# Kernel optimization log

Hardware: AMD Instinct MI355X
Metric: run time of the kernel (lower is better)

## Reference

```python
import jax, jax.numpy as jnp
import numpy as np

B, T, E = 2, 2048, 1024
H = 16
D = E // H  # 64

def setup_inputs() -> dict:
    key = jax.random.key(0)
    kx, kq, kk, kv, ko = jax.random.split(key, 5)
    s = 1.0 / np.sqrt(E)
    return {
        "x":  jax.random.normal(kx, (B, T, E), dtype=jnp.float32),
        "Wq": jax.random.normal(kq, (E, E), dtype=jnp.float32) * s,
        "Wk": jax.random.normal(kk, (E, E), dtype=jnp.float32) * s,
        "Wv": jax.random.normal(kv, (E, E), dtype=jnp.float32) * s,
        "Wo": jax.random.normal(ko, (E, E), dtype=jnp.float32) * s,
    }

def reference(x, Wq, Wk, Wv, Wo):
    # Faithful to the torch module, including its quirks:
    #  - head split is a raw .view(B, H, T, D) reshape (NOT a transpose split)
    #  - masked_fill result is discarded in the original, so NO causal mask is applied
    #  - dropout = 0.0 -> identity
    b, t, e = x.shape
    q = jnp.reshape(x @ Wq, (b, H, t, D))
    k = jnp.reshape(x @ Wk, (b, H, t, D))
    v = jnp.reshape(x @ Wv, (b, H, t, D))
    # raw_score = q @ k^T ; softmax over keys of raw_score / sqrt(head_dim)
    scores = jnp.einsum("bhtd,bhsd->bhts", q, k) / jnp.sqrt(jnp.asarray(D, x.dtype))
    attn = jax.nn.softmax(scores, axis=-1)
    h = jnp.einsum("bhts,bhsd->bhtd", attn, v)           # (B,H,T,D)
    h = jnp.reshape(h, (b, t, e))                         # .view(B, T, -1)
    return h @ Wo
```

## Files before the change

### kernel.cpp

```cpp
#include <hip/hip_runtime.h>
#include <hip/hip_bf16.h>
#include <math.h>

#define BB 2
#define TT 2048
#define EE 1024
#define HH 16
#define DD 64
#define MM (BB*TT)

typedef __bf16 bf16;
typedef bf16 bf16x8 __attribute__((ext_vector_type(8)));
typedef bf16 bf16x4 __attribute__((ext_vector_type(4)));
typedef bf16 bf16x2 __attribute__((ext_vector_type(2)));
typedef float f32x4 __attribute__((ext_vector_type(4)));

#define MFMA16(a,b,c) __builtin_amdgcn_mfma_f32_16x16x32_bf16((a),(b),(c),0,0,0)

__device__ __forceinline__ void gload_lds16(const void* g, void* l) {
  __builtin_amdgcn_global_load_lds(
      (const __attribute__((address_space(1))) unsigned int*)g,
      (__attribute__((address_space(3))) unsigned int*)l, 16, 0, 0);
}

__device__ __forceinline__ unsigned short bits(bf16 h) {
  return __builtin_bit_cast(unsigned short, h);
}

__global__ __launch_bounds__(256) void cvt_bf16(const float* __restrict__ in,
                                                bf16* __restrict__ out, int n4) {
  int i = blockIdx.x * blockDim.x + threadIdx.x;
  if (i < n4) {
    float4 f = ((const float4*)in)[i];
    bf16x4 h;
    h[0] = (bf16)f.x; h[1] = (bf16)f.y; h[2] = (bf16)f.z; h[3] = (bf16)f.w;
    ((bf16x4*)out)[i] = h;
  }
}

__global__ __launch_bounds__(256) void transpose_cvt4(const float* __restrict__ w0,
                                                      const float* __restrict__ w1,
                                                      const float* __restrict__ w2,
                                                      const float* __restrict__ w3,
                                                      bf16* t0, bf16* t1, bf16* t2, bf16* t3) {
  const float* W = blockIdx.z == 0 ? w0 : blockIdx.z == 1 ? w1 : blockIdx.z == 2 ? w2 : w3;
  bf16* T = blockIdx.z == 0 ? t0 : blockIdx.z == 1 ? t1 : blockIdx.z == 2 ? t2 : t3;
  __shared__ bf16 tile[64][65];
  const int n0 = blockIdx.x * 64, k0 = blockIdx.y * 64;
#pragma unroll
  for (int i = 0; i < 16; i++) {
    int idx = threadIdx.x + i * 256;
    int r = idx >> 6, c = idx & 63;
    tile[c][r] = (bf16)W[(size_t)(k0 + r) * EE + n0 + c];
  }
  __syncthreads();
#pragma unroll
  for (int i = 0; i < 16; i++) {
    int idx = threadIdx.x + i * 256;
    int r = idx >> 6, c = idx & 63;
    T[(size_t)(n0 + r) * EE + k0 + c] = tile[r][c];
  }
}

template <typename OutT>
__device__ __forceinline__ void gemm_core(const bf16* __restrict__ A, const bf16* __restrict__ Bt,
                                          OutT* __restrict__ C, bf16* As, bf16* Bs) {
  const int tid = threadIdx.x;
  const int w = tid >> 6, lane = tid & 63;
  const int lg = lane >> 4, lr = lane & 15;
  const int row0 = blockIdx.y * 128, col0 = blockIdx.x * 128;
  const int wrow = (w >> 1) * 64, wcol = (w & 1) * 64;
  f32x4 acc[4][4];
#pragma unroll
  for (int m = 0; m < 4; m++)
#pragma unroll
    for (int n = 0; n < 4; n++) acc[m][n] = f32x4{0.f, 0.f, 0.f, 0.f};

  for (int kt = 0; kt < EE; kt += 32) {
#pragma unroll
    for (int i = 0; i < 2; i++) {
      const int c = i * 4 + w;
      const int row = c * 16 + (lane >> 2);
      const int kof = (lane & 3) * 8;
      gload_lds16(A + (size_t)(row0 + row) * EE + kt + kof, &As[c * 512]);
      gload_lds16(Bt + (size_t)(col0 + row) * EE + kt + kof, &Bs[c * 512]);
    }
    __syncthreads();
    bf16x8 a[4], b[4];
#pragma unroll
    for (int m = 0; m < 4; m++)
      a[m] = *(const bf16x8*)&As[(wrow + m * 16 + lr) * 32 + lg * 8];
#pragma unroll
    for (int n = 0; n < 4; n++)
      b[n] = *(const bf16x8*)&Bs[(wcol + n * 16 + lr) * 32 + lg * 8];
#pragma unroll
    for (int m = 0; m < 4; m++)
#pragma unroll
      for (int n = 0; n < 4; n++) acc[m][n] = MFMA16(a[m], b[n], acc[m][n]);
    __syncthreads();
  }
#pragma unroll
  for (int m = 0; m < 4; m++)
#pragma unroll
    for (int n = 0; n < 4; n++)
#pragma unroll
      for (int r = 0; r < 4; r++) {
        const int rr = row0 + wrow + m * 16 + lg * 4 + r;
        const int cc = col0 + wcol + n * 16 + lr;
        C[(size_t)rr * EE + cc] = (OutT)acc[m][n][r];
      }
}

__global__ __launch_bounds__(256) void gemm_qkv(const bf16* __restrict__ A,
                                                const bf16* __restrict__ w0,
                                                const bf16* __restrict__ w1,
                                                const bf16* __restrict__ w2,
                                                bf16* o0, bf16* o1, bf16* o2) {
  __shared__ __align__(16) bf16 As[128 * 32];
  __shared__ __align__(16) bf16 Bs[128 * 32];
  const bf16* Bt = (blockIdx.z == 0) ? w0 : (blockIdx.z == 1) ? w1 : w2;
  bf16* C = (blockIdx.z == 0) ? o0 : (blockIdx.z == 1) ? o1 : o2;
  gemm_core<bf16>(A, Bt, C, As, Bs);
}

__global__ __launch_bounds__(256) void gemm_out(const bf16* __restrict__ A,
                                                const bf16* __restrict__ Bt,
                                                float* __restrict__ C) {
  __shared__ __align__(16) bf16 As[128 * 32];
  __shared__ __align__(16) bf16 Bs[128 * 32];
  gemm_core<float>(A, Bt, C, As, Bs);
}

__global__ __launch_bounds__(512, 4) void flash_attn(const bf16* __restrict__ Q,
                                                     const bf16* __restrict__ K,
                                                     const bf16* __restrict__ V,
                                                     bf16* __restrict__ Hout) {
  const int tid = threadIdx.x;
  const int w = tid >> 6, lane = tid & 63;
  const int hi = lane >> 4, lr = lane & 15;

  const int bid = blockIdx.x + 16 * blockIdx.y;
  const int sid = (bid & 7) * 64 + (bid >> 3);
  const int qb = sid & 15, bh = sid >> 4;

  const size_t base = (size_t)(bh >> 4) * TT * EE + (size_t)(bh & 15) * 128 * EE;
  const bf16* qh = Q + base;
  const bf16* kh = K + base;
  const bf16* vh = V + base;
  bf16* hh = Hout + base;
  const int r0w = qb * 128 + w * 16;

  __shared__ __align__(16) bf16 Ks[2][64 * 72];
  __shared__ __align__(16) bf16 Vt[2][64 * 72];
  __shared__ __align__(16) bf16 Ps[8 * 16 * 72];
  bf16* Pw = &Ps[w * 16 * 72];

  const float qscale = 0.18033688011112042f;
  bf16x8 aq[2];
#pragma unroll
  for (int kk = 0; kk < 2; kk++) {
    bf16x8 qv = *(const bf16x8*)(qh + (size_t)(r0w + lr) * DD + kk * 32 + hi * 8);
#pragma unroll
    for (int j = 0; j < 8; j++) qv[j] = (bf16)(qscale * (float)qv[j]);
    aq[kk] = qv;
  }

  float l_ = 0.f;
  f32x4 o[4];
#pragma unroll
  for (int d = 0; d < 4; d++) o[d] = f32x4{0.f, 0.f, 0.f, 0.f};

  const int ks_s = tid >> 3, ks_d = (tid & 7) * 8;
  const int vsp = tid & 31, vdb = (tid >> 5) * 4;

  bf16x8 kreg = *(const bf16x8*)(kh + (size_t)ks_s * DD + ks_d);
  bf16x4 va = *(const bf16x4*)(vh + (size_t)(2 * vsp) * DD + vdb);
  bf16x4 vb2 = *(const bf16x4*)(vh + (size_t)(2 * vsp + 1) * DD + vdb);
  *(bf16x8*)&Ks[0][ks_s * 72 + ks_d] = kreg;
#pragma unroll
  for (int j = 0; j < 4; j++) {
    unsigned u = (unsigned)bits(va[j]) | ((unsigned)bits(vb2[j]) << 16);
    *(unsigned*)&Vt[0][(vdb + j) * 72 + 2 * vsp] = u;
  }
  kreg = *(const bf16x8*)(kh + (size_t)(64 + ks_s) * DD + ks_d);
  va = *(const bf16x4*)(vh + (size_t)(64 + 2 * vsp) * DD + vdb);
  vb2 = *(const bf16x4*)(vh + (size_t)(64 + 2 * vsp + 1) * DD + vdb);
  __syncthreads();

  for (int t = 0; t < TT / 64; t++) {
    const bf16* Kc = Ks[t & 1];
    const bf16* Vc = Vt[t & 1];

    f32x4 sA[4];
#pragma unroll
    for (int cf = 0; cf < 4; cf++) sA[cf] = f32x4{0.f, 0.f, 0.f, 0.f};
#pragma unroll
    for (int cf = 0; cf < 4; cf++)
#pragma unroll
      for (int kk = 0; kk < 2; kk++) {
        bf16x8 bk = *(const bf16x8*)&Kc[(cf * 16 + lr) * 72 + kk * 32 + hi * 8];
        sA[cf] = MFMA16(bk, aq[kk], sA[cf]);
      }

#pragma unroll
    for (int cf = 0; cf < 4; cf++) {
      bf16x4 pb;
#pragma unroll
      for (int r = 0; r < 4; r++) {
        float p = __builtin_amdgcn_exp2f(sA[cf][r]);
        l_ += p;
        pb[r] = (bf16)p;
      }
      *(bf16x4*)&Pw[lr * 72 + cf * 16 + 4 * hi] = pb;
    }
    asm volatile("s_waitcnt lgkmcnt(0)" ::: "memory");

#pragma unroll
    for (int kk = 0; kk < 2; kk++) {
      bf16x8 bp = *(const bf16x8*)&Pw[lr * 72 + kk * 32 + hi * 8];
#pragma unroll
      for (int dblk = 0; dblk < 4; dblk++) {
        bf16x8 av = *(const bf16x8*)&Vc[(dblk * 16 + lr) * 72 + kk * 32 + hi * 8];
        o[dblk] = MFMA16(av, bp, o[dblk]);
      }
    }

    if (t < TT / 64 - 1) {
      bf16* Kn = Ks[(t + 1) & 1];
      bf16* Vn = Vt[(t + 1) & 1];
      *(bf16x8*)&Kn[ks_s * 72 + ks_d] = kreg;
#pragma unroll
      for (int j = 0; j < 4; j++) {
        unsigned u = (unsigned)bits(va[j]) | ((unsigned)bits(vb2[j]) << 16);
        *(unsigned*)&Vn[(vdb + j) * 72 + 2 * vsp] = u;
      }
      if (t < TT / 64 - 2) {
        const int s2 = (t + 2) * 64;
        kreg = *(const bf16x8*)(kh + (size_t)(s2 + ks_s) * DD + ks_d);
        va = *(const bf16x4*)(vh + (size_t)(s2 + 2 * vsp) * DD + vdb);
        vb2 = *(const bf16x4*)(vh + (size_t)(s2 + 2 * vsp + 1) * DD + vdb);
      }
    }
    __syncthreads();
  }

  float lt = l_;
  lt += __shfl_xor(lt, 16);
  lt += __shfl_xor(lt, 32);
#pragma unroll
  for (int dblk = 0; dblk < 4; dblk++) {
    bf16x4 st;
#pragma unroll
    for (int r = 0; r < 4; r++) st[r] = (bf16)(o[dblk][r] / lt);
    *(bf16x4*)(hh + (size_t)(r0w + lr) * DD + dblk * 16 + 4 * hi) = st;
  }
}

extern "C" void kernel_launch(void* const* d_in, const int* in_sizes, int n_in,
                              void* d_out, int out_size, void* d_ws, size_t ws_size,
                              hipStream_t stream) {
  const float* x  = (const float*)d_in[0];
  const float* Wq = (const float*)d_in[1];
  const float* Wk = (const float*)d_in[2];
  const float* Wv = (const float*)d_in[3];
  const float* Wo = (const float*)d_in[4];
  float* out = (float*)d_out;

  bf16* xb  = (bf16*)d_ws;
  bf16* wqt = xb + (size_t)MM * EE;
  bf16* wkt = wqt + (size_t)EE * EE;
  bf16* wvt = wkt + (size_t)EE * EE;
  bf16* wot = wvt + (size_t)EE * EE;
  bf16* Qb  = wot + (size_t)EE * EE;
  bf16* Kb  = Qb + (size_t)MM * EE;
  bf16* Vb  = Kb + (size_t)MM * EE;
  bf16* Hb  = xb;

  cvt_bf16<<<dim3(MM * EE / 1024), 256, 0, stream>>>(x, xb, MM * EE / 4);
  transpose_cvt4<<<dim3(16, 16, 4), 256, 0, stream>>>(Wq, Wk, Wv, Wo, wqt, wkt, wvt, wot);
  gemm_qkv<<<dim3(8, 32, 3), 256, 0, stream>>>(xb, wqt, wkt, wvt, Qb, Kb, Vb);
  flash_attn<<<dim3(16, 32), 512, 0, stream>>>(Qb, Kb, Vb, Hb);
  gemm_out<<<dim3(8, 32), 256, 0, stream>>>(Hb, wot, out);
}
```

Before: 126.7 us.

## Double-buffer GEMM LDS tiles, remap GEMM blocks, and reorder attention PV after prefetch

The GEMM core now double-buffers its LDS tiles, issuing the next K-slice's global-to-LDS loads before computing on the current one, which removes one barrier per iteration. The QKV and output GEMMs use a 1D grid with a swizzled block-to-tile mapping, relying on the contiguous Wq/Wk/Wv/Qb/Kb/Vb workspace layout. In flash attention, the PV MFMAs move after the next K/V tile is written to LDS, the row-sum is accumulated vectorially, and the final divide becomes a reciprocal multiply. Doubling LDS per GEMM block may reduce occupancy, and the single-buffer synchronisation in attention gets more sensitive to ordering.

```diff
diff --git a/kernel.cpp b/kernel.cpp
--- a/kernel.cpp
+++ b/kernel.cpp
@@ -12,7 +12,6 @@
 typedef __bf16 bf16;
 typedef bf16 bf16x8 __attribute__((ext_vector_type(8)));
 typedef bf16 bf16x4 __attribute__((ext_vector_type(4)));
-typedef bf16 bf16x2 __attribute__((ext_vector_type(2)));
 typedef float f32x4 __attribute__((ext_vector_type(4)));
 
 #define MFMA16(a,b,c) __builtin_amdgcn_mfma_f32_16x16x32_bf16((a),(b),(c),0,0,0)
@@ -63,42 +62,59 @@
 }
 
 template <typename OutT>
-__device__ __forceinline__ void gemm_core(const bf16* __restrict__ A, const bf16* __restrict__ Bt,
-                                          OutT* __restrict__ C, bf16* As, bf16* Bs) {
+__device__ __forceinline__ void gemm_core2(const bf16* __restrict__ A,
+                                           const bf16* __restrict__ Bt_tile,
+                                           OutT* __restrict__ C, size_t ldc,
+                                           int row0, int colc,
+                                           bf16* As, bf16* Bs) {
   const int tid = threadIdx.x;
   const int w = tid >> 6, lane = tid & 63;
   const int lg = lane >> 4, lr = lane & 15;
-  const int row0 = blockIdx.y * 128, col0 = blockIdx.x * 128;
   const int wrow = (w >> 1) * 64, wcol = (w & 1) * 64;
+  const int srow = (tid >> 2) & 15;
+  const int kof = (lane & 3) * 8;
+
   f32x4 acc[4][4];
 #pragma unroll
   for (int m = 0; m < 4; m++)
 #pragma unroll
     for (int n = 0; n < 4; n++) acc[m][n] = f32x4{0.f, 0.f, 0.f, 0.f};
 
-  for (int kt = 0; kt < EE; kt += 32) {
-#pragma unroll
-    for (int i = 0; i < 2; i++) {
-      const int c = i * 4 + w;
-      const int row = c * 16 + (lane >> 2);
-      const int kof = (lane & 3) * 8;
-      gload_lds16(A + (size_t)(row0 + row) * EE + kt + kof, &As[c * 512]);
-      gload_lds16(Bt + (size_t)(col0 + row) * EE + kt + kof, &Bs[c * 512]);
-    }
-    __syncthreads();
+#define G_STAGE(buf, kt)                                                         \
+  {                                                                              \
+    _Pragma("unroll") for (int i = 0; i < 2; i++) {                              \
+      const int c = i * 4 + w;                                                   \
+      const int row = c * 16 + srow;                                             \
+      gload_lds16(A + (size_t)(row0 + row) * EE + (kt) + kof,                    \
+                  &As[(buf) * 4096 + c * 512]);                                  \
+      gload_lds16(Bt_tile + (size_t)row * EE + (kt) + kof,                       \
+                  &Bs[(buf) * 4096 + c * 512]);                                  \
+    }                                                                            \
+  }
+
+  G_STAGE(0, 0);
+  __syncthreads();
+
+  for (int kt = 0; kt < 32; kt++) {
+    const int cur = kt & 1;
+    if (kt < 31) G_STAGE(cur ^ 1, (kt + 1) * 32);
+    const bf16* Ac = &As[cur * 4096];
+    const bf16* Bc = &Bs[cur * 4096];
     bf16x8 a[4], b[4];
 #pragma unroll
     for (int m = 0; m < 4; m++)
-      a[m] = *(const bf16x8*)&As[(wrow + m * 16 + lr) * 32 + lg * 8];
+      a[m] = *(const bf16x8*)&Ac[(wrow + m * 16 + lr) * 32 + lg * 8];
 #pragma unroll
     for (int n = 0; n < 4; n++)
-      b[n] = *(const bf16x8*)&Bs[(wcol + n * 16 + lr) * 32 + lg * 8];
+      b[n] = *(const bf16x8*)&Bc[(wcol + n * 16 + lr) * 32 + lg * 8];
 #pragma unroll
     for (int m = 0; m < 4; m++)
 #pragma unroll
       for (int n = 0; n < 4; n++) acc[m][n] = MFMA16(a[m], b[n], acc[m][n]);
     __syncthreads();
   }
+#undef G_STAGE
+
 #pragma unroll
   for (int m = 0; m < 4; m++)
 #pragma unroll
@@ -106,29 +122,36 @@
 #pragma unroll
       for (int r = 0; r < 4; r++) {
         const int rr = row0 + wrow + m * 16 + lg * 4 + r;
-        const int cc = col0 + wcol + n * 16 + lr;
-        C[(size_t)rr * EE + cc] = (OutT)acc[m][n][r];
+        const int cc = colc + wcol + n * 16 + lr;
+        C[(size_t)rr * ldc + cc] = (OutT)acc[m][n][r];
       }
 }
 
 __global__ __launch_bounds__(256) void gemm_qkv(const bf16* __restrict__ A,
-                                                const bf16* __restrict__ w0,
-                                                const bf16* __restrict__ w1,
-                                                const bf16* __restrict__ w2,
-                                                bf16* o0, bf16* o1, bf16* o2) {
-  __shared__ __align__(16) bf16 As[128 * 32];
-  __shared__ __align__(16) bf16 Bs[128 * 32];
-  const bf16* Bt = (blockIdx.z == 0) ? w0 : (blockIdx.z == 1) ? w1 : w2;
-  bf16* C = (blockIdx.z == 0) ? o0 : (blockIdx.z == 1) ? o1 : o2;
-  gemm_core<bf16>(A, Bt, C, As, Bs);
+                                                const bf16* __restrict__ BtAll,
+                                                bf16* __restrict__ OutAll) {
+  __shared__ __align__(16) bf16 As[2 * 128 * 32];
+  __shared__ __align__(16) bf16 Bs[2 * 128 * 32];
+  const int bid = blockIdx.x;
+  const int sid = (bid & 7) * 96 + (bid >> 3);
+  const int rowt = sid & 31, colt = sid >> 5;
+  const int col0 = colt * 128;
+  const int mat = col0 >> 10;
+  bf16* Cb = OutAll + (size_t)mat * MM * EE;
+  gemm_core2<bf16>(A, BtAll + (size_t)col0 * EE, Cb, EE,
+                   rowt * 128, col0 & 1023, As, Bs);
 }
 
 __global__ __launch_bounds__(256) void gemm_out(const bf16* __restrict__ A,
                                                 const bf16* __restrict__ Bt,
                                                 float* __restrict__ C) {
-  __shared__ __align__(16) bf16 As[128 * 32];
-  __shared__ __align__(16) bf16 Bs[128 * 32];
-  gemm_core<float>(A, Bt, C, As, Bs);
+  __shared__ __align__(16) bf16 As[2 * 128 * 32];
+  __shared__ __align__(16) bf16 Bs[2 * 128 * 32];
+  const int bid = blockIdx.x;
+  const int sid = (bid & 7) * 32 + (bid >> 3);
+  const int rowt = sid & 31, colt = sid >> 5;
+  gemm_core2<float>(A, Bt + (size_t)(colt * 128) * EE, C, EE,
+                    rowt * 128, colt * 128, As, Bs);
 }
 
 __global__ __launch_bounds__(512, 4) void flash_attn(const bf16* __restrict__ Q,
@@ -165,7 +188,7 @@
     aq[kk] = qv;
   }
 
-  float l_ = 0.f;
+  f32x4 lacc = f32x4{0.f, 0.f, 0.f, 0.f};
   f32x4 o[4];
 #pragma unroll
   for (int d = 0; d < 4; d++) o[d] = f32x4{0.f, 0.f, 0.f, 0.f};
@@ -202,27 +225,18 @@
         sA[cf] = MFMA16(bk, aq[kk], sA[cf]);
       }
 
+    f32x4 pv[4];
+#pragma unroll
+    for (int cf = 0; cf < 4; cf++)
+#pragma unroll
+      for (int r = 0; r < 4; r++) pv[cf][r] = __builtin_amdgcn_exp2f(sA[cf][r]);
+    lacc += (pv[0] + pv[1]) + (pv[2] + pv[3]);
 #pragma unroll
     for (int cf = 0; cf < 4; cf++) {
       bf16x4 pb;
 #pragma unroll
-      for (int r = 0; r < 4; r++) {
-        float p = __builtin_amdgcn_exp2f(sA[cf][r]);
-        l_ += p;
-        pb[r] = (bf16)p;
-      }
+      for (int r = 0; r < 4; r++) pb[r] = (bf16)pv[cf][r];
       *(bf16x4*)&Pw[lr * 72 + cf * 16 + 4 * hi] = pb;
-    }
-    asm volatile("s_waitcnt lgkmcnt(0)" ::: "memory");
-
-#pragma unroll
-    for (int kk = 0; kk < 2; kk++) {
-      bf16x8 bp = *(const bf16x8*)&Pw[lr * 72 + kk * 32 + hi * 8];
-#pragma unroll
-      for (int dblk = 0; dblk < 4; dblk++) {
-        bf16x8 av = *(const bf16x8*)&Vc[(dblk * 16 + lr) * 72 + kk * 32 + hi * 8];
-        o[dblk] = MFMA16(av, bp, o[dblk]);
-      }
     }
 
     if (t < TT / 64 - 1) {
@@ -241,17 +255,29 @@
         vb2 = *(const bf16x4*)(vh + (size_t)(s2 + 2 * vsp + 1) * DD + vdb);
       }
     }
+    asm volatile("s_waitcnt lgkmcnt(0)" ::: "memory");
+
+#pragma unroll
+    for (int kk = 0; kk < 2; kk++) {
+      bf16x8 bp = *(const bf16x8*)&Pw[lr * 72 + kk * 32 + hi * 8];
+#pragma unroll
+      for (int dblk = 0; dblk < 4; dblk++) {
+        bf16x8 av = *(const bf16x8*)&Vc[(dblk * 16 + lr) * 72 + kk * 32 + hi * 8];
+        o[dblk] = MFMA16(av, bp, o[dblk]);
+      }
+    }
     __syncthreads();
   }
 
-  float lt = l_;
+  float lt = (lacc[0] + lacc[1]) + (lacc[2] + lacc[3]);
   lt += __shfl_xor(lt, 16);
   lt += __shfl_xor(lt, 32);
+  const float inv = __builtin_amdgcn_rcpf(lt);
 #pragma unroll
   for (int dblk = 0; dblk < 4; dblk++) {
     bf16x4 st;
 #pragma unroll
-    for (int r = 0; r < 4; r++) st[r] = (bf16)(o[dblk][r] / lt);
+    for (int r = 0; r < 4; r++) st[r] = (bf16)(o[dblk][r] * inv);
     *(bf16x4*)(hh + (size_t)(r0w + lr) * DD + dblk * 16 + 4 * hi) = st;
   }
 }
@@ -278,7 +304,7 @@
 
   cvt_bf16<<<dim3(MM * EE / 1024), 256, 0, stream>>>(x, xb, MM * EE / 4);
   transpose_cvt4<<<dim3(16, 16, 4), 256, 0, stream>>>(Wq, Wk, Wv, Wo, wqt, wkt, wvt, wot);
-  gemm_qkv<<<dim3(8, 32, 3), 256, 0, stream>>>(xb, wqt, wkt, wvt, Qb, Kb, Vb);
+  gemm_qkv<<<dim3(768), 256, 0, stream>>>(xb, wqt, Qb);
   flash_attn<<<dim3(16, 32), 512, 0, stream>>>(Qb, Kb, Vb, Hb);
-  gemm_out<<<dim3(8, 32), 256, 0, stream>>>(Hb, wot, out);
-}
+  gemm_out<<<dim3(256), 256, 0, stream>>>(Hb, wot, out);
+}
```

New measurement: 137.2 us. 1.08x slower.
